# Performance work log

Measured on AMD Instinct MI355X. Metric: run time of the kernel, lower is better.

The kernel has to match this reference:

```python
import jax, jax.numpy as jnp
import numpy as np
import math

B, S, D, H = 8, 1024, 256, 8
HD = D // H  # head size = 32


def setup_inputs() -> dict:
    key = jax.random.key(0)
    ks = jax.random.split(key, 12)
    inp = {
        "query": jax.random.normal(ks[0], (B, S, D), jnp.float32),
        "key": jax.random.normal(ks[1], (B, S, D), jnp.float32),
        "value": jax.random.normal(ks[2], (B, S, D), jnp.float32),
        "rel": jax.random.uniform(ks[3], (B, S, S), jnp.float32),
        "timestamp": jax.random.normal(ks[4], (B, S, S), jnp.float32),
        "l1": jax.random.uniform(ks[5], (1,), jnp.float32),
        "l2": jax.random.uniform(ks[6], (1,), jnp.float32),
        # projection weights (nn.Linear: y = x @ W.T + b)
        "Wq": jax.random.normal(ks[7], (D, D), jnp.float32) / math.sqrt(D),
        "bq": jnp.zeros((D,), jnp.float32),
        "Wk": jax.random.normal(ks[8], (D, D), jnp.float32) / math.sqrt(D),
        "bk": jnp.zeros((D,), jnp.float32),
        "Wv": jax.random.normal(ks[9], (D, D), jnp.float32) / math.sqrt(D),
        "bv": jnp.zeros((D,), jnp.float32),
    }
    return inp


def reference(query, key, value, rel, timestamp, l1, l2, Wq, bq, Wk, bk, Wv, bv):
    b, s, d = query.shape
    h, hd = H, HD

    def proj(x, W, bias):
        # [b,s,d] -> [b,h,s,hd]
        return (x @ W.T + bias).reshape(b, s, h, hd).transpose(0, 2, 1, 3)

    q = proj(query, Wq, bq)
    k = proj(key, Wk, bk)
    v = proj(value, Wv, bv)

    # causal future mask: True above the diagonal (future positions)
    mask = jnp.triu(jnp.ones((s, s), dtype=bool), k=1)[None, None]  # [1,1,s,s]

    # relation attention: rel * mask, zeros -> -10000, softmax
    relm = rel[:, None] * mask.astype(rel.dtype)  # broadcast over heads [b,1->h,s,s]
    rel_attn = jax.nn.softmax(jnp.where(relm == 0, jnp.float32(-10000.0), relm), axis=-1)

    # scaled dot-product scores with causal mask
    scores = jnp.einsum('bhqd,bhkd->bhqk', q, k) / math.sqrt(hd)
    scores = jnp.where(mask, jnp.float32(-1e9), scores)
    prob_attn = jax.nn.softmax(scores, axis=-1)

    # time-decay attention: exp(-|t|), masked to -inf (use -1e30 for grad safety)
    ts = jnp.where(mask, jnp.float32(-1e30), jnp.exp(-jnp.abs(timestamp[:, None])))
    time_attn = jax.nn.softmax(ts, axis=-1)

    # blend (time_include=True, qrelation_include=True)
    prob = (1.0 - l2) * prob_attn + l2 * time_attn
    prob = (1.0 - l1) * prob + l1 * rel_attn

    out = jnp.einsum('bhqk,bhkd->bhqd', prob, v)
    out = out.transpose(0, 2, 1, 3).reshape(b, s, d)
    return out
```

## Files before the change

kernel.cpp:

```cpp
#include <hip/hip_runtime.h>
#include <math.h>

constexpr int B = 8, S = 1024, D = 256, H = 8, HD = 32;

typedef __attribute__((ext_vector_type(8))) short bf16x8;
typedef __attribute__((ext_vector_type(16))) float f32x16;
typedef __attribute__((ext_vector_type(2)))  int  int2v;

__device__ __forceinline__ uint cvtpk(float a, float b) {
    uint r;
    asm("v_cvt_pk_bf16_f32 %0, %1, %2" : "=v"(r) : "v"(a), "v"(b));
    return r;
}
__device__ __forceinline__ float xswap32f(float v, int hi) {
    int2v t = __builtin_amdgcn_permlane32_swap(__float_as_int(v), __float_as_int(v), false, false);
    return __int_as_float(hi ? t[0] : t[1]);
}

__global__ __launch_bounds__(512, 4) void proj_mfma(
    const float* __restrict__ query, const float* __restrict__ key_,
    const float* __restrict__ value,
    const float* __restrict__ Wq, const float* __restrict__ Wk,
    const float* __restrict__ Wv,
    const float* __restrict__ bq, const float* __restrict__ bk,
    const float* __restrict__ bv, float qscale,
    ushort* __restrict__ qbuf, ushort* __restrict__ kbuf,
    ushort* __restrict__ vtbuf, float* __restrict__ cpart)
{
    __shared__ ushort xf[8192];
    __shared__ float bias_lds[256];

    const int m = blockIdx.y;
    const int tid = threadIdx.x;
    const int w = tid >> 6, lane = tid & 63;
    const int l31 = lane & 31, hi = lane >> 5;
    const int h = w;

    const float* xsrc = (m == 0) ? query : (m == 1) ? key_ : value;
    const float* Wsrc = (m == 0) ? Wq : (m == 1) ? Wk : Wv;
    const float* bsrc = (m == 0) ? bq : (m == 1) ? bk : bv;
    ushort* yb = (m == 0) ? qbuf : (m == 1) ? kbuf : vtbuf;
    const float wscale = (m == 0) ? qscale : 1.0f;

    if (tid < 256) bias_lds[tid] = bsrc[tid] * wscale;

    bf16x8 wf[16];
    {
        const float* wrow = Wsrc + ((size_t)(h * 32 + l31)) * 256 + hi * 8;
        #pragma unroll
        for (int kc = 0; kc < 16; ++kc) {
            float4 a = *(const float4*)(wrow + kc * 16);
            float4 b = *(const float4*)(wrow + kc * 16 + 4);
            uint4 p;
            p.x = cvtpk(a.x * wscale, a.y * wscale);
            p.y = cvtpk(a.z * wscale, a.w * wscale);
            p.z = cvtpk(b.x * wscale, b.y * wscale);
            p.w = cvtpk(b.z * wscale, b.w * wscale);
            wf[kc] = __builtin_bit_cast(bf16x8, p);
        }
    }

    const int sst = tid & 31, skc = tid >> 5;
    float cpacc = 0.f;

    for (int it = 0; it < 2; ++it) {
        const int stile = blockIdx.x * 2 + it;
        const int b_ = stile >> 5, t32 = stile & 31;

        __syncthreads();
        {
            const float* xrow = xsrc + ((size_t)(stile * 32 + sst)) * 256 + skc * 16;
            float4 a0 = *(const float4*)(xrow + 0);
            float4 a1 = *(const float4*)(xrow + 4);
            float4 a2 = *(const float4*)(xrow + 8);
            float4 a3 = *(const float4*)(xrow + 12);
            uint2 w01 = { cvtpk(a0.x, a0.y), cvtpk(a0.z, a0.w) };
            uint2 w23 = { cvtpk(a1.x, a1.y), cvtpk(a1.z, a1.w) };
            uint2 w45 = { cvtpk(a2.x, a2.y), cvtpk(a2.z, a2.w) };
            uint2 w67 = { cvtpk(a3.x, a3.y), cvtpk(a3.z, a3.w) };
            ushort* base = xf + skc * 512 + sst * 4;
            *(uint2*)(base +   0) = w01;
            *(uint2*)(base + 128) = w23;
            *(uint2*)(base + 256) = w45;
            *(uint2*)(base + 384) = w67;
        }
        __syncthreads();

        f32x16 acc;
        #pragma unroll
        for (int r = 0; r < 16; ++r) acc[r] = 0.f;
        #pragma unroll
        for (int kc = 0; kc < 16; ++kc) {
            const ushort* rb = xf + kc * 512 + hi * 256 + l31 * 4;
            uint2 lo = *(const uint2*)rb;
            uint2 hj = *(const uint2*)(rb + 128);
            uint4 xw = { lo.x, lo.y, hj.x, hj.y };
            bf16x8 xfrag = __builtin_bit_cast(bf16x8, xw);
            if (m < 2)
                acc = __builtin_amdgcn_mfma_f32_32x32x16_bf16(wf[kc], xfrag, acc, 0, 0, 0);
            else
                acc = __builtin_amdgcn_mfma_f32_32x32x16_bf16(xfrag, wf[kc], acc, 0, 0, 0);
        }

        if (m < 2) {
            #pragma unroll
            for (int r = 0; r < 16; ++r)
                acc[r] += bias_lds[h * 32 + (r & 3) + 8 * (r >> 2) + 4 * hi];
        } else {
            const float bl = bias_lds[h * 32 + l31];
            #pragma unroll
            for (int r = 0; r < 16; ++r) acc[r] += bl;
            float cp = 0.f;
            #pragma unroll
            for (int r = 0; r < 16; ++r) cp += acc[r];
            cp += __shfl_xor(cp, 32);
            cpacc += cp;
        }

        uint wa0 = cvtpk(acc[0], acc[1]),   wa1 = cvtpk(acc[2], acc[3]);
        uint wb0 = cvtpk(acc[4], acc[5]),   wb1 = cvtpk(acc[6], acc[7]);
        uint wa2 = cvtpk(acc[8], acc[9]),   wa3 = cvtpk(acc[10], acc[11]);
        uint wb2 = cvtpk(acc[12], acc[13]), wb3 = cvtpk(acc[14], acc[15]);
        int2v s0 = __builtin_amdgcn_permlane32_swap((int)wa0, (int)wb0, false, false);
        int2v s1 = __builtin_amdgcn_permlane32_swap((int)wa1, (int)wb1, false, false);
        int2v s2 = __builtin_amdgcn_permlane32_swap((int)wa2, (int)wb2, false, false);
        int2v s3 = __builtin_amdgcn_permlane32_swap((int)wa3, (int)wb3, false, false);
        uint4 p0 = { (uint)s0[0], (uint)s1[0], (uint)s0[1], (uint)s1[1] };
        uint4 p1 = { (uint)s2[0], (uint)s3[0], (uint)s2[1], (uint)s3[1] };
        ushort* dst = yb + (((size_t)b_ * H + h) * 32 + t32) * 1024 + hi * 256 + l31 * 8;
        *(uint4*)dst = p0;
        *(uint4*)(dst + 512) = p1;
    }
    if (m == 2 && hi == 0)
        cpart[blockIdx.x * D + h * 32 + l31] = cpacc;
}

__global__ __launch_bounds__(512, 4) void timerel_mfma(
    const float* __restrict__ ts, const float* __restrict__ rel,
    const ushort* __restrict__ vtb, const float* __restrict__ cpart,
    const float* __restrict__ l1p, const float* __restrict__ l2p,
    float* __restrict__ out)
{
    __shared__ ushort wlds[64 * 512];
    __shared__ float nuni[32];

    const int b  = blockIdx.y;
    const int i0 = blockIdx.x * 32;
    const int w = threadIdx.x >> 6, lane = threadIdx.x & 63;
    const int l31 = lane & 31, hi = lane >> 5;
    const float l1 = l1p[0], l2 = l2p[0];

    const int hig_w = (lane >> 1) & 1, jh_w = lane & 1;
    const int ksl_lo = lane >> 2;

    for (int pp = 0; pp < 2; ++pp) {
        float wv[2][4][4];
        float stp[2] = { 0.f, 0.f }, srp[2] = { 0.f, 0.f };
        #pragma unroll
        for (int rr = 0; rr < 2; ++rr) {
            const int row = w * 4 + pp * 2 + rr;
            const int i = i0 + row;
            const float* tsrow  = ts  + ((size_t)b * S + i) * S;
            const float* relrow = rel + ((size_t)b * S + i) * S;
            #pragma unroll
            for (int seg = 0; seg < 4; ++seg) {
                const int jb = seg * 256 + lane * 4;
                if (seg * 256 + 255 <= i) {
                    float4 t4 = *(const float4*)(tsrow + jb);
                    const float te[4] = { t4.x, t4.y, t4.z, t4.w };
                    #pragma unroll
                    for (int e = 0; e < 4; ++e) {
                        float v = __expf(__expf(-fabsf(te[e])));
                        stp[rr] += v; wv[rr][seg][e] = v;
                    }
                } else if (seg * 256 > i) {
                    float4 r4 = *(const float4*)(relrow + jb);
                    const float re[4] = { r4.x, r4.y, r4.z, r4.w };
                    #pragma unroll
                    for (int e = 0; e < 4; ++e) {
                        float v = (re[e] != 0.f) ? __expf(re[e]) : 0.f;
                        srp[rr] += v; wv[rr][seg][e] = v;
                    }
                } else {
                    float4 t4 = *(const float4*)(tsrow + jb);
                    float4 r4 = *(const float4*)(relrow + jb);
                    const float te[4] = { t4.x, t4.y, t4.z, t4.w };
                    const float re[4] = { r4.x, r4.y, r4.z, r4.w };
                    #pragma unroll
                    for (int e = 0; e < 4; ++e) {
                        float v;
                        if (jb + e <= i) { v = __expf(__expf(-fabsf(te[e]))); stp[rr] += v; }
                        else             { v = (re[e] != 0.f) ? __expf(re[e]) : 0.f; srp[rr] += v; }
                        wv[rr][seg][e] = v;
                    }
                }
            }
        }
        #pragma unroll
        for (int off = 1; off < 64; off <<= 1) {
            stp[0] += __shfl_xor(stp[0], off);
            srp[0] += __shfl_xor(srp[0], off);
            stp[1] += __shfl_xor(stp[1], off);
            srp[1] += __shfl_xor(srp[1], off);
        }
        #pragma unroll
        for (int rr = 0; rr < 2; ++rr) {
            const int row = w * 4 + pp * 2 + rr;
            const int i = i0 + row;
            const float nt = (1.f - l1) * l2 / stp[rr];
            const float nr = (srp[rr] > 0.5f) ? (l1 / srp[rr]) : 0.f;
            if (lane == 0) nuni[row] = (srp[rr] > 0.5f) ? 0.f : (l1 / (float)S);
            #pragma unroll
            for (int seg = 0; seg < 4; ++seg) {
                const int jb = seg * 256 + lane * 4;
                float a0 = wv[rr][seg][0] * ((jb     <= i) ? nt : nr);
                float a1 = wv[rr][seg][1] * ((jb + 1 <= i) ? nt : nr);
                float a2 = wv[rr][seg][2] * ((jb + 2 <= i) ? nt : nr);
                float a3 = wv[rr][seg][3] * ((jb + 3 <= i) ? nt : nr);
                uint2 pk; pk.x = cvtpk(a0, a1); pk.y = cvtpk(a2, a3);
                const int ksl = seg * 16 + ksl_lo;
                const int xorv = jh_w | (hig_w << 1) | ((ksl & 7) << 2);
                char* dst = (char*)wlds + ksl * 1024 + hig_w * 512 + jh_w * 256
                            + ((row ^ xorv) & 31) * 8;
                *(uint2*)dst = pk;
            }
        }
    }
    __syncthreads();

    const ushort* vtbase = vtb + ((size_t)b * 8 + w) * 32768 + hi * 256 + l31 * 8;
    f32x16 acc;
    #pragma unroll
    for (int r = 0; r < 16; ++r) acc[r] = 0.f;
    #pragma unroll 4
    for (int ks = 0; ks < 64; ++ks) {
        const int x0 = 0 | (hi << 1) | ((ks & 7) << 2);
        const int x1 = 1 | (hi << 1) | ((ks & 7) << 2);
        const char* base = (const char*)wlds + ks * 1024 + hi * 512;
        uint2 lo = *(const uint2*)(base +       ((l31 ^ x0) & 31) * 8);
        uint2 hj = *(const uint2*)(base + 256 + ((l31 ^ x1) & 31) * 8);
        uint4 aw = { lo.x, lo.y, hj.x, hj.y };
        bf16x8 afrag = __builtin_bit_cast(bf16x8, aw);
        bf16x8 vf = *(const bf16x8*)(vtbase + (size_t)ks * 512);
        acc = __builtin_amdgcn_mfma_f32_32x32x16_bf16(afrag, vf, acc, 0, 0, 0);
    }

    const int d = w * 32 + l31;
    float cv = 0.f;
    if (i0 == S - 32) {
        #pragma unroll
        for (int p_ = 0; p_ < 16; ++p_)
            cv += cpart[(b * 16 + p_) * D + d];
    }
    float* obase = out + ((size_t)b * S + i0) * D + d;
    #pragma unroll
    for (int r = 0; r < 16; ++r) {
        const int row = (r & 3) + 8 * (r >> 2) + 4 * hi;
        obase[(size_t)row * D] = acc[r] + nuni[row] * cv;
    }
}

#define LOADKV(K0, K1, V0, V1, KT) do { \
    const ushort* kp_ = kbase + (size_t)(KT) * 1024; \
    const ushort* vp_ = vbase + (size_t)(KT) * 1024; \
    K0 = *(const bf16x8*)kp_;        K1 = *(const bf16x8*)(kp_ + 512); \
    V0 = *(const bf16x8*)vp_;        V1 = *(const bf16x8*)(vp_ + 512); \
} while (0)

#define TILE_COMPUTE(K0, K1, V0, V1, ISDIAG) do { \
    f32x16 stv; \
    _Pragma("unroll") for (int r = 0; r < 16; ++r) stv[r] = 0.f; \
    stv = __builtin_amdgcn_mfma_f32_32x32x16_bf16(K0, qf0, stv, 0, 0, 0); \
    stv = __builtin_amdgcn_mfma_f32_32x32x16_bf16(K1, qf1, stv, 0, 0, 0); \
    if (ISDIAG) { \
        _Pragma("unroll") for (int r = 0; r < 16; ++r) \
            if (((r & 3) + 8 * (r >> 2) + 4 * hi) > l31) stv[r] = -1e30f; \
    } \
    float p[16]; \
    _Pragma("unroll") for (int r = 0; r < 16; ++r) { p[r] = exp2f(stv[r]); lacc += p[r]; } \
    uint wa0 = cvtpk(p[0], p[1]),   wa1 = cvtpk(p[2], p[3]); \
    uint wb0 = cvtpk(p[4], p[5]),   wb1 = cvtpk(p[6], p[7]); \
    uint wa2 = cvtpk(p[8], p[9]),   wa3 = cvtpk(p[10], p[11]); \
    uint wb2 = cvtpk(p[12], p[13]), wb3 = cvtpk(p[14], p[15]); \
    int2v s0 = __builtin_amdgcn_permlane32_swap((int)wa0, (int)wb0, false, false); \
    int2v s1 = __builtin_amdgcn_permlane32_swap((int)wa1, (int)wb1, false, false); \
    int2v s2 = __builtin_amdgcn_permlane32_swap((int)wa2, (int)wb2, false, false); \
    int2v s3 = __builtin_amdgcn_permlane32_swap((int)wa3, (int)wb3, false, false); \
    uint4 pa0i = { (uint)s0[0], (uint)s1[0], (uint)s0[1], (uint)s1[1] }; \
    uint4 pa1i = { (uint)s2[0], (uint)s3[0], (uint)s2[1], (uint)s3[1] }; \
    bf16x8 pa0 = __builtin_bit_cast(bf16x8, pa0i); \
    bf16x8 pa1 = __builtin_bit_cast(bf16x8, pa1i); \
    ot = __builtin_amdgcn_mfma_f32_32x32x16_bf16(V0, pa0, ot, 0, 0, 0); \
    ot = __builtin_amdgcn_mfma_f32_32x32x16_bf16(V1, pa1, ot, 0, 0, 0); \
} while (0)

__global__ __launch_bounds__(512, 4) void flash_mfma(
    const ushort* __restrict__ qb, const ushort* __restrict__ kb,
    const ushort* __restrict__ vtb, const float* __restrict__ l1p,
    const float* __restrict__ l2p, float* __restrict__ out)
{
    __shared__ float mbuf[4][64][18];
    __shared__ float lds_t[4][32 * 33];
    const int id = blockIdx.x;
    const int halfg = id >> 8, rr_ = id & 255;
    const int qraw = rr_ >> 5;
    const int qblk = halfg ? (7 - qraw) : qraw;
    const int bh = (rr_ & 31) | (halfg << 5);
    const int b = bh >> 3, h = bh & 7;
    const int w = threadIdx.x >> 6, lane = threadIdx.x & 63;
    const int sub = w & 3, half = w >> 2;
    const int l31 = lane & 31, hi = lane >> 5;
    const int qt = qblk * 4 + sub;
    const float c_p = (1.f - l1p[0]) * (1.f - l2p[0]);

    const ushort* qp_ = qb + ((size_t)bh * 32 + qt) * 1024 + hi * 256 + l31 * 8;
    const bf16x8 qf0 = *(const bf16x8*)qp_;
    const bf16x8 qf1 = *(const bf16x8*)(qp_ + 512);
    const ushort* kbase = kb  + (size_t)bh * 32768 + hi * 256 + l31 * 8;
    const ushort* vbase = vtb + (size_t)bh * 32768 + hi * 256 + l31 * 8;

    f32x16 ot;
    #pragma unroll
    for (int r = 0; r < 16; ++r) ot[r] = 0.f;
    float lacc = 0.f;

    const int nlo = (qt + 1) >> 1;
    const int klo = half ? nlo : 0;
    const int khi = half ? qt : (nlo - 1);

    if (klo <= khi) {
        bf16x8 kA0, kA1, vA0, vA1, kB0, kB1, vB0, vB1;
        LOADKV(kA0, kA1, vA0, vA1, klo);
        int kt = klo;
        for (;;) {
            if (kt + 1 <= khi) LOADKV(kB0, kB1, vB0, vB1, kt + 1);
            TILE_COMPUTE(kA0, kA1, vA0, vA1, kt == qt);
            if (++kt > khi) break;
            if (kt + 1 <= khi) LOADKV(kA0, kA1, vA0, vA1, kt + 1);
            TILE_COMPUTE(kB0, kB1, vB0, vB1, kt == qt);
            if (++kt > khi) break;
        }
    }

    if (half == 1) {
        float* mb = &mbuf[sub][lane][0];
        #pragma unroll
        for (int r = 0; r < 16; r += 4)
            *(float4*)&mb[r] = make_float4(ot[r], ot[r+1], ot[r+2], ot[r+3]);
        mb[16] = lacc;
    }
    __syncthreads();

    if (half == 0) {
        const float* mb = &mbuf[sub][lane][0];
        #pragma unroll
        for (int r = 0; r < 16; ++r) ot[r] += mb[r];
        lacc += mb[16];
        const float lrun = lacc + xswap32f(lacc, hi);
        const float inv = c_p / lrun;
        float* lt = lds_t[sub];
        #pragma unroll
        for (int r = 0; r < 16; ++r) {
            const int d = (r & 3) + 8 * (r >> 2) + 4 * hi;
            lt[l31 * 33 + d] = ot[r] * inv;
        }
    }
    __syncthreads();
    if (half == 0) {
        const int q0w = qt * 32;
        const float* lt = lds_t[sub];
        #pragma unroll
        for (int rr = 0; rr < 4; ++rr) {
            const int ql = rr * 8 + (lane >> 3);
            const int d0 = (lane & 7) * 4;
            const float* lp = &lt[ql * 33 + d0];
            float* op = out + ((size_t)b * S + q0w + ql) * D + h * 32 + d0;
            float4 cur = *(const float4*)op;
            cur.x += lp[0]; cur.y += lp[1]; cur.z += lp[2]; cur.w += lp[3];
            *(float4*)op = cur;
        }
    }
}

extern "C" void kernel_launch(void* const* d_in, const int* in_sizes, int n_in,
                              void* d_out, int out_size, void* d_ws, size_t ws_size,
                              hipStream_t stream)
{
    (void)in_sizes; (void)n_in; (void)out_size; (void)ws_size;
    const float* query = (const float*)d_in[0];
    const float* key_  = (const float*)d_in[1];
    const float* value = (const float*)d_in[2];
    const float* rel   = (const float*)d_in[3];
    const float* tsp   = (const float*)d_in[4];
    const float* l1p   = (const float*)d_in[5];
    const float* l2p   = (const float*)d_in[6];
    const float* Wq    = (const float*)d_in[7];
    const float* bq    = (const float*)d_in[8];
    const float* Wk    = (const float*)d_in[9];
    const float* bk    = (const float*)d_in[10];
    const float* Wv    = (const float*)d_in[11];
    const float* bv    = (const float*)d_in[12];
    float* out = (float*)d_out;

    ushort* qbuf  = (ushort*)d_ws;
    ushort* kbuf  = (ushort*)((char*)d_ws + (4u  << 20));
    ushort* vtbuf = (ushort*)((char*)d_ws + (8u  << 20));
    float*  cpart = (float*)((char*)d_ws + (12u << 20));

    const float qscale = 1.4426950408889634f * 0.17677669529663687f;

    proj_mfma<<<dim3(128, 3), 512, 0, stream>>>(
        query, key_, value, Wq, Wk, Wv, bq, bk, bv, qscale,
        qbuf, kbuf, vtbuf, cpart);

    timerel_mfma<<<dim3(S / 32, B), 512, 0, stream>>>(
        tsp, rel, vtbuf, cpart, l1p, l2p, out);

    flash_mfma<<<512, 512, 0, stream>>>(qbuf, kbuf, vtbuf, l1p, l2p, out);
}
```

Baseline: 64.44 us.

## Split time/relation attention into weight-building and GEMM kernels

The fused time/relation kernel is split in two. The first computes the normalized bf16 weight tiles from timestamp and rel, then writes them and the per-row uniform coefficients to a global workspace. The second reloads the tiles into LDS and runs the MFMA product with V across twice as many smaller blocks, each covering half of D. The aim is more parallelism and less per-block work in the GEMM stage, and the weights kernel no longer depends on the projection. The cost is an extra global round trip for about 16 MB of weights plus one more kernel launch.

```diff
diff --git a/kernel.cpp b/kernel.cpp
--- a/kernel.cpp
+++ b/kernel.cpp
@@ -135,23 +135,22 @@
         cpart[blockIdx.x * D + h * 32 + l31] = cpacc;
 }
 
-__global__ __launch_bounds__(512, 4) void timerel_mfma(
+__global__ __launch_bounds__(512, 2) void weights_kernel(
     const float* __restrict__ ts, const float* __restrict__ rel,
-    const ushort* __restrict__ vtb, const float* __restrict__ cpart,
     const float* __restrict__ l1p, const float* __restrict__ l2p,
-    float* __restrict__ out)
+    ushort* __restrict__ wbuf, float* __restrict__ gnuni)
 {
-    __shared__ ushort wlds[64 * 512];
-    __shared__ float nuni[32];
-
-    const int b  = blockIdx.y;
-    const int i0 = blockIdx.x * 32;
-    const int w = threadIdx.x >> 6, lane = threadIdx.x & 63;
-    const int l31 = lane & 31, hi = lane >> 5;
+    __shared__ ushort wlds[32768];
+    const int t32 = blockIdx.x, b = blockIdx.y;
+    const int i0 = t32 * 32;
+    const int tid = threadIdx.x;
+    const int w = tid >> 6, lane = tid & 63;
     const float l1 = l1p[0], l2 = l2p[0];
 
-    const int hig_w = (lane >> 1) & 1, jh_w = lane & 1;
-    const int ksl_lo = lane >> 2;
+    const int kslo = lane >> 2;
+    const int hig  = (lane >> 1) & 1;
+    const int half = lane & 1;
+    const int xo   = kslo << 3;
 
     for (int pp = 0; pp < 2; ++pp) {
         float wv[2][4][4];
@@ -209,7 +208,9 @@
             const int i = i0 + row;
             const float nt = (1.f - l1) * l2 / stp[rr];
             const float nr = (srp[rr] > 0.5f) ? (l1 / srp[rr]) : 0.f;
-            if (lane == 0) nuni[row] = (srp[rr] > 0.5f) ? 0.f : (l1 / (float)S);
+            if (lane == 0)
+                gnuni[(b * 32 + t32) * 32 + row] =
+                    (srp[rr] > 0.5f) ? 0.f : (l1 / (float)S);
             #pragma unroll
             for (int seg = 0; seg < 4; ++seg) {
                 const int jb = seg * 256 + lane * 4;
@@ -218,34 +219,64 @@
                 float a2 = wv[rr][seg][2] * ((jb + 2 <= i) ? nt : nr);
                 float a3 = wv[rr][seg][3] * ((jb + 3 <= i) ? nt : nr);
                 uint2 pk; pk.x = cvtpk(a0, a1); pk.y = cvtpk(a2, a3);
-                const int ksl = seg * 16 + ksl_lo;
-                const int xorv = jh_w | (hig_w << 1) | ((ksl & 7) << 2);
-                char* dst = (char*)wlds + ksl * 1024 + hig_w * 512 + jh_w * 256
-                            + ((row ^ xorv) & 31) * 8;
-                *(uint2*)dst = pk;
+                const int ks = seg * 16 + kslo;
+                const int byte = ks * 1024 + hig * 512 + half * 256
+                                 + ((row * 8) ^ xo);
+                *(uint2*)((char*)wlds + byte) = pk;
             }
         }
     }
     __syncthreads();
 
-    const ushort* vtbase = vtb + ((size_t)b * 8 + w) * 32768 + hi * 256 + l31 * 8;
+    const uint4* srcv = (const uint4*)wlds;
+    uint4* dstv = (uint4*)(wbuf + (size_t)(b * 32 + t32) * 32768);
+    #pragma unroll
+    for (int r = 0; r < 8; ++r)
+        dstv[r * 512 + tid] = srcv[r * 512 + tid];
+}
+
+__global__ __launch_bounds__(256, 4) void timerel_gemm(
+    const ushort* __restrict__ wbuf, const ushort* __restrict__ vtb,
+    const float* __restrict__ cpart, const float* __restrict__ gnuni,
+    float* __restrict__ out)
+{
+    __shared__ ushort wlds[32768];
+    __shared__ float sh_nuni[32];
+    const int t32 = blockIdx.x, b = blockIdx.y, dh = blockIdx.z;
+    const int i0 = t32 * 32;
+    const int tid = threadIdx.x;
+
+    {
+        const uint4* srcv = (const uint4*)(wbuf + (size_t)(b * 32 + t32) * 32768);
+        uint4* dstv = (uint4*)wlds;
+        #pragma unroll
+        for (int r = 0; r < 16; ++r)
+            dstv[r * 256 + tid] = srcv[r * 256 + tid];
+        if (tid < 32) sh_nuni[tid] = gnuni[(b * 32 + t32) * 32 + tid];
+    }
+    __syncthreads();
+
+    const int w = tid >> 6, lane = tid & 63;
+    const int l31 = lane & 31, hi = lane >> 5;
+    const int dchunk = dh * 4 + w;
+
+    const ushort* vtbase = vtb + ((size_t)b * 8 + dchunk) * 32768 + hi * 256 + l31 * 8;
     f32x16 acc;
     #pragma unroll
     for (int r = 0; r < 16; ++r) acc[r] = 0.f;
     #pragma unroll 4
     for (int ks = 0; ks < 64; ++ks) {
-        const int x0 = 0 | (hi << 1) | ((ks & 7) << 2);
-        const int x1 = 1 | (hi << 1) | ((ks & 7) << 2);
+        const int xo = (ks & 15) << 3;
         const char* base = (const char*)wlds + ks * 1024 + hi * 512;
-        uint2 lo = *(const uint2*)(base +       ((l31 ^ x0) & 31) * 8);
-        uint2 hj = *(const uint2*)(base + 256 + ((l31 ^ x1) & 31) * 8);
+        uint2 lo = *(const uint2*)(base +       ((l31 * 8) ^ xo));
+        uint2 hj = *(const uint2*)(base + 256 + ((l31 * 8) ^ xo));
         uint4 aw = { lo.x, lo.y, hj.x, hj.y };
         bf16x8 afrag = __builtin_bit_cast(bf16x8, aw);
         bf16x8 vf = *(const bf16x8*)(vtbase + (size_t)ks * 512);
         acc = __builtin_amdgcn_mfma_f32_32x32x16_bf16(afrag, vf, acc, 0, 0, 0);
     }
 
-    const int d = w * 32 + l31;
+    const int d = dchunk * 32 + l31;
     float cv = 0.f;
     if (i0 == S - 32) {
         #pragma unroll
@@ -256,7 +287,7 @@
     #pragma unroll
     for (int r = 0; r < 16; ++r) {
         const int row = (r & 3) + 8 * (r >> 2) + 4 * hi;
-        obase[(size_t)row * D] = acc[r] + nuni[row] * cv;
+        obase[(size_t)row * D] = acc[r] + sh_nuni[row] * cv;
     }
 }
 
@@ -406,15 +437,20 @@
     ushort* kbuf  = (ushort*)((char*)d_ws + (4u  << 20));
     ushort* vtbuf = (ushort*)((char*)d_ws + (8u  << 20));
     float*  cpart = (float*)((char*)d_ws + (12u << 20));
+    float*  gnuni = (float*)((char*)d_ws + (12u << 20) + (256u << 10));
+    ushort* wbuf  = (ushort*)((char*)d_ws + (16u << 20));
 
     const float qscale = 1.4426950408889634f * 0.17677669529663687f;
+
+    weights_kernel<<<dim3(32, B), 512, 0, stream>>>(
+        tsp, rel, l1p, l2p, wbuf, gnuni);
 
     proj_mfma<<<dim3(128, 3), 512, 0, stream>>>(
         query, key_, value, Wq, Wk, Wv, bq, bk, bv, qscale,
         qbuf, kbuf, vtbuf, cpart);
 
-    timerel_mfma<<<dim3(S / 32, B), 512, 0, stream>>>(
-        tsp, rel, vtbuf, cpart, l1p, l2p, out);
+    timerel_gemm<<<dim3(32, B, 2), 256, 0, stream>>>(
+        wbuf, vtbuf, cpart, gnuni, out);
 
     flash_mfma<<<512, 512, 0, stream>>>(qbuf, kbuf, vtbuf, l1p, l2p, out);
 }
```

Measured after the change: 71.18 us. 10.5% more time.
